# Kernel tuning notes

Hardware: AMD Instinct MI355X
Metric: run time of the kernel (lower is better)

Reference implementation:

```python
import jax, jax.numpy as jnp
import numpy as np


def _make_hadamard(n: int) -> np.ndarray:
    # Sylvester construction; H is symmetric so H == H.T
    H = np.array([[1.0]], dtype=np.float32)
    while H.shape[0] < n:
        H = np.block([[H, H], [H, -H]])
    return H


def setup_inputs() -> dict:
    key = jax.random.key(0)
    k1, k2, k3 = jax.random.split(key, 3)
    B, L, N = 64, 4096, 512  # N = num_features = num_features_pad (power of 2)
    x = jax.random.normal(k1, (B, L, N), dtype=jnp.float32)
    v = jax.random.uniform(k2, (N,), dtype=jnp.float32)  # torch.rand init
    T = jax.random.uniform(k3, (N,), dtype=jnp.float32)  # SoftThresholding threshold
    return {"x": x, "v": v, "T": T}


def reference(x, v, T):
    n = x.shape[-1]
    H = jnp.asarray(_make_hadamard(n))  # [n, n], symmetric
    scale = np.float32(1.0 / np.sqrt(n))
    # normalized Hadamard transform along last axis (dense-GEMM form, H.T == H)
    f1 = (x @ H) * scale
    # per-feature gate
    f2 = v * f1
    # soft-threshold: sign(x) * relu(|x| - T)
    f3 = jnp.sign(f2) * jax.nn.relu(jnp.abs(f2) - T)
    # inverse (same normalized) transform
    f4 = (f3 @ H) * scale
    # no padding (n is a power of 2), slice is identity; residual add
    return f4 + x
```

## Files before the change

### kernel.cpp

```cpp
#include <hip/hip_runtime.h>

#define NF 512
#define SCALE 0.044194173824159216f

#if defined(__has_builtin)
#  if __has_builtin(__builtin_amdgcn_permlane32_swap)
#    define HAVE_PL32 1
#  else
#    define HAVE_PL32 0
#  endif
#  if __has_builtin(__builtin_amdgcn_permlane16_swap)
#    define HAVE_PL16 1
#  else
#    define HAVE_PL16 0
#  endif
#else
#  define HAVE_PL32 0
#  define HAVE_PL16 0
#endif

typedef unsigned uint2v __attribute__((ext_vector_type(2)));
typedef float f32x4 __attribute__((ext_vector_type(4)));

template<int CTRL>
__device__ __forceinline__ float dppf(float x) {
    const int xi = __float_as_int(x);
    return __int_as_float(__builtin_amdgcn_update_dpp(xi, xi, CTRL, 0xF, 0xF, true));
}

template<int PAT>
__device__ __forceinline__ float swzf(float x) {
    return __int_as_float(__builtin_amdgcn_ds_swizzle(__float_as_int(x), PAT));
}

#if HAVE_PL16
__device__ __forceinline__ void bfly16(float& a, float& b) {
    uint2v t = __builtin_amdgcn_permlane16_swap(__float_as_uint(a), __float_as_uint(b), false, false);
    const float lo = __uint_as_float(t[0]);
    const float hi = __uint_as_float(t[1]);
    const float s = lo + hi;
    const float d = lo - hi;
    uint2v u = __builtin_amdgcn_permlane16_swap(__float_as_uint(s), __float_as_uint(d), false, false);
    a = __uint_as_float(u[0]);
    b = __uint_as_float(u[1]);
}
#endif

#if HAVE_PL32
__device__ __forceinline__ void bfly32(float& a, float& b) {
    uint2v t = __builtin_amdgcn_permlane32_swap(__float_as_uint(a), __float_as_uint(b), false, false);
    const float lo = __uint_as_float(t[0]);
    const float hi = __uint_as_float(t[1]);
    const float s = lo + hi;
    const float d = lo - hi;
    uint2v u = __builtin_amdgcn_permlane32_swap(__float_as_uint(s), __float_as_uint(d), false, false);
    a = __uint_as_float(u[0]);
    b = __uint_as_float(u[1]);
}
#endif

__device__ __forceinline__ void wht512(float r[8], const float sg1, const float sg2,
                                       const float sg4, const float sg8, const float sg16,
                                       const float sg32) {
    (void)sg16; (void)sg32;
#pragma unroll
    for (int s = 1; s < 8; s <<= 1) {
#pragma unroll
        for (int j = 0; j < 8; ++j) {
            if (!(j & s)) {
                const float u = r[j], w = r[j | s];
                r[j] = u + w;
                r[j | s] = u - w;
            }
        }
    }
#pragma unroll
    for (int j = 0; j < 8; ++j) { const float p = dppf<0xB1>(r[j]); r[j] = fmaf(sg1, r[j], p); }
#pragma unroll
    for (int j = 0; j < 8; ++j) { const float p = dppf<0x4E>(r[j]); r[j] = fmaf(sg2, r[j], p); }
#pragma unroll
    for (int j = 0; j < 8; ++j) { const float p = swzf<0x101F>(r[j]); r[j] = fmaf(sg4, r[j], p); }
#pragma unroll
    for (int j = 0; j < 8; ++j) { const float p = dppf<0x128>(r[j]); r[j] = fmaf(sg8, r[j], p); }
#if HAVE_PL16
#pragma unroll
    for (int j = 0; j < 8; j += 2) bfly16(r[j], r[j + 1]);
#else
#pragma unroll
    for (int j = 0; j < 8; ++j) { const float p = swzf<0x401F>(r[j]); r[j] = fmaf(sg16, r[j], p); }
#endif
#if HAVE_PL32
#pragma unroll
    for (int j = 0; j < 8; j += 2) bfly32(r[j], r[j + 1]);
#else
#pragma unroll
    for (int j = 0; j < 8; ++j) { const float p = __shfl_xor(r[j], 32, 64); r[j] = fmaf(sg32, r[j], p); }
#endif
}

__global__ __launch_bounds__(256, 4)
void wht512_soft_kernel(const float* __restrict__ x,
                        const float* __restrict__ gate,
                        const float* __restrict__ thr,
                        float* __restrict__ out,
                        const int nrows) {
    const int lane = threadIdx.x & 63;
    const int wave = blockIdx.x * (blockDim.x >> 6) + (threadIdx.x >> 6);
    const int nwaves = gridDim.x * (blockDim.x >> 6);

    const float sg1  = (lane & 1)  ? -1.0f : 1.0f;
    const float sg2  = (lane & 2)  ? -1.0f : 1.0f;
    const float sg4  = (lane & 4)  ? -1.0f : 1.0f;
    const float sg8  = (lane & 8)  ? -1.0f : 1.0f;
    const float sg16 = (lane & 16) ? -1.0f : 1.0f;
    const float sg32 = (lane & 32) ? -1.0f : 1.0f;

    float vg[8], tg[8];
    {
        const f32x4 a = ((const f32x4*)gate)[lane * 2];
        const f32x4 b = ((const f32x4*)gate)[lane * 2 + 1];
        vg[0] = a.x * SCALE; vg[1] = a.y * SCALE; vg[2] = a.z * SCALE; vg[3] = a.w * SCALE;
        vg[4] = b.x * SCALE; vg[5] = b.y * SCALE; vg[6] = b.z * SCALE; vg[7] = b.w * SCALE;
        const f32x4 c = ((const f32x4*)thr)[lane * 2];
        const f32x4 d = ((const f32x4*)thr)[lane * 2 + 1];
        tg[0] = c.x; tg[1] = c.y; tg[2] = c.z; tg[3] = c.w;
        tg[4] = d.x; tg[5] = d.y; tg[6] = d.z; tg[7] = d.w;
    }

    int row = wave;
    f32x4 ca, cb;
    if (row < nrows) {
        const f32x4* xr = (const f32x4*)(x + (size_t)row * NF);
        ca = __builtin_nontemporal_load(&xr[lane * 2]);
        cb = __builtin_nontemporal_load(&xr[lane * 2 + 1]);
    }

    for (; row < nrows; row += nwaves) {
        const int nrow = row + nwaves;
        f32x4 na = ca, nb = cb;
        if (nrow < nrows) {
            const f32x4* xn = (const f32x4*)(x + (size_t)nrow * NF);
            na = __builtin_nontemporal_load(&xn[lane * 2]);
            nb = __builtin_nontemporal_load(&xn[lane * 2 + 1]);
        }

        float r[8] = {ca.x, ca.y, ca.z, ca.w, cb.x, cb.y, cb.z, cb.w};

        wht512(r, sg1, sg2, sg4, sg8, sg16, sg32);

#pragma unroll
        for (int j = 0; j < 8; ++j) {
            const float f = r[j] * vg[j];
            const float mdiff = fabsf(f) - tg[j];
            r[j] = (mdiff > 0.0f) ? copysignf(mdiff, f) : 0.0f;
        }

        wht512(r, sg1, sg2, sg4, sg8, sg16, sg32);

        f32x4 oa, ob;
        oa.x = fmaf(r[0], SCALE, ca.x);
        oa.y = fmaf(r[1], SCALE, ca.y);
        oa.z = fmaf(r[2], SCALE, ca.z);
        oa.w = fmaf(r[3], SCALE, ca.w);
        ob.x = fmaf(r[4], SCALE, cb.x);
        ob.y = fmaf(r[5], SCALE, cb.y);
        ob.z = fmaf(r[6], SCALE, cb.z);
        ob.w = fmaf(r[7], SCALE, cb.w);
        f32x4* orow = (f32x4*)(out + (size_t)row * NF);
        __builtin_nontemporal_store(oa, &orow[lane * 2]);
        __builtin_nontemporal_store(ob, &orow[lane * 2 + 1]);

        ca = na;
        cb = nb;
    }
}

extern "C" void kernel_launch(void* const* d_in, const int* in_sizes, int n_in,
                              void* d_out, int out_size, void* d_ws, size_t ws_size,
                              hipStream_t stream) {
    const float* x = (const float*)d_in[0];
    const float* v = (const float*)d_in[1];
    const float* T = (const float*)d_in[2];
    float* out = (float*)d_out;

    const int nrows = in_sizes[0] / NF;

    dim3 block(256);
    dim3 grid(4096);
    hipLaunchKernelGGL(wht512_soft_kernel, grid, block, 0, stream, x, v, T, out, nrows);
}
```

Measured before the change: 235.1 us.

## Process two rows per wave with interleaved butterflies and plain loads/stores

Each wave now handles a pair of adjacent rows and interleaves their Hadamard butterfly and cross-lane stages. This raises instruction-level parallelism, hides DPP/permlane latency, and doubles the bytes in flight per wave. Nontemporal loads and stores are also replaced with ordinary ones. The cost is higher register pressure, and an odd final row would be dropped, though the row count here is even.

```diff
diff --git a/kernel.cpp b/kernel.cpp
--- a/kernel.cpp
+++ b/kernel.cpp
@@ -59,42 +59,74 @@
 }
 #endif
 
-__device__ __forceinline__ void wht512(float r[8], const float sg1, const float sg2,
-                                       const float sg4, const float sg8, const float sg16,
-                                       const float sg32) {
+__device__ __forceinline__ void wht512_pair(float a[8], float b[8],
+                                            const float sg1, const float sg2,
+                                            const float sg4, const float sg8,
+                                            const float sg16, const float sg32) {
     (void)sg16; (void)sg32;
 #pragma unroll
     for (int s = 1; s < 8; s <<= 1) {
 #pragma unroll
         for (int j = 0; j < 8; ++j) {
             if (!(j & s)) {
-                const float u = r[j], w = r[j | s];
-                r[j] = u + w;
-                r[j | s] = u - w;
+                const float ua = a[j], wa = a[j | s];
+                const float ub = b[j], wb = b[j | s];
+                a[j] = ua + wa; a[j | s] = ua - wa;
+                b[j] = ub + wb; b[j | s] = ub - wb;
             }
         }
     }
 #pragma unroll
-    for (int j = 0; j < 8; ++j) { const float p = dppf<0xB1>(r[j]); r[j] = fmaf(sg1, r[j], p); }
-#pragma unroll
-    for (int j = 0; j < 8; ++j) { const float p = dppf<0x4E>(r[j]); r[j] = fmaf(sg2, r[j], p); }
-#pragma unroll
-    for (int j = 0; j < 8; ++j) { const float p = swzf<0x101F>(r[j]); r[j] = fmaf(sg4, r[j], p); }
-#pragma unroll
-    for (int j = 0; j < 8; ++j) { const float p = dppf<0x128>(r[j]); r[j] = fmaf(sg8, r[j], p); }
+    for (int j = 0; j < 8; ++j) {
+        const float pa = dppf<0xB1>(a[j]);
+        const float pb = dppf<0xB1>(b[j]);
+        a[j] = fmaf(sg1, a[j], pa);
+        b[j] = fmaf(sg1, b[j], pb);
+    }
+#pragma unroll
+    for (int j = 0; j < 8; ++j) {
+        const float pa = dppf<0x4E>(a[j]);
+        const float pb = dppf<0x4E>(b[j]);
+        a[j] = fmaf(sg2, a[j], pa);
+        b[j] = fmaf(sg2, b[j], pb);
+    }
+#pragma unroll
+    for (int j = 0; j < 8; ++j) {
+        const float pa = swzf<0x101F>(a[j]);
+        const float pb = swzf<0x101F>(b[j]);
+        a[j] = fmaf(sg4, a[j], pa);
+        b[j] = fmaf(sg4, b[j], pb);
+    }
+#pragma unroll
+    for (int j = 0; j < 8; ++j) {
+        const float pa = dppf<0x128>(a[j]);
+        const float pb = dppf<0x128>(b[j]);
+        a[j] = fmaf(sg8, a[j], pa);
+        b[j] = fmaf(sg8, b[j], pb);
+    }
 #if HAVE_PL16
 #pragma unroll
-    for (int j = 0; j < 8; j += 2) bfly16(r[j], r[j + 1]);
+    for (int j = 0; j < 8; j += 2) { bfly16(a[j], a[j + 1]); bfly16(b[j], b[j + 1]); }
 #else
 #pragma unroll
-    for (int j = 0; j < 8; ++j) { const float p = swzf<0x401F>(r[j]); r[j] = fmaf(sg16, r[j], p); }
+    for (int j = 0; j < 8; ++j) {
+        const float pa = swzf<0x401F>(a[j]);
+        const float pb = swzf<0x401F>(b[j]);
+        a[j] = fmaf(sg16, a[j], pa);
+        b[j] = fmaf(sg16, b[j], pb);
+    }
 #endif
 #if HAVE_PL32
 #pragma unroll
-    for (int j = 0; j < 8; j += 2) bfly32(r[j], r[j + 1]);
+    for (int j = 0; j < 8; j += 2) { bfly32(a[j], a[j + 1]); bfly32(b[j], b[j + 1]); }
 #else
 #pragma unroll
-    for (int j = 0; j < 8; ++j) { const float p = __shfl_xor(r[j], 32, 64); r[j] = fmaf(sg32, r[j], p); }
+    for (int j = 0; j < 8; ++j) {
+        const float pa = __shfl_xor(a[j], 32, 64);
+        const float pb = __shfl_xor(b[j], 32, 64);
+        a[j] = fmaf(sg32, a[j], pa);
+        b[j] = fmaf(sg32, b[j], pb);
+    }
 #endif
 }
 
@@ -107,6 +139,7 @@
     const int lane = threadIdx.x & 63;
     const int wave = blockIdx.x * (blockDim.x >> 6) + (threadIdx.x >> 6);
     const int nwaves = gridDim.x * (blockDim.x >> 6);
+    const int npairs = nrows >> 1;
 
     const float sg1  = (lane & 1)  ? -1.0f : 1.0f;
     const float sg2  = (lane & 2)  ? -1.0f : 1.0f;
@@ -127,51 +160,61 @@
         tg[4] = d.x; tg[5] = d.y; tg[6] = d.z; tg[7] = d.w;
     }
 
-    int row = wave;
-    f32x4 ca, cb;
-    if (row < nrows) {
-        const f32x4* xr = (const f32x4*)(x + (size_t)row * NF);
-        ca = __builtin_nontemporal_load(&xr[lane * 2]);
-        cb = __builtin_nontemporal_load(&xr[lane * 2 + 1]);
-    }
-
-    for (; row < nrows; row += nwaves) {
-        const int nrow = row + nwaves;
-        f32x4 na = ca, nb = cb;
-        if (nrow < nrows) {
-            const f32x4* xn = (const f32x4*)(x + (size_t)nrow * NF);
-            na = __builtin_nontemporal_load(&xn[lane * 2]);
-            nb = __builtin_nontemporal_load(&xn[lane * 2 + 1]);
+    int pr = wave;
+    f32x4 c0a, c0b, c1a, c1b;
+    if (pr < npairs) {
+        const f32x4* x0 = (const f32x4*)(x + (size_t)(2 * pr) * NF);
+        c0a = x0[lane * 2];
+        c0b = x0[lane * 2 + 1];
+        c1a = x0[128 + lane * 2];
+        c1b = x0[128 + lane * 2 + 1];
+    }
+
+    for (; pr < npairs; pr += nwaves) {
+        const int npr = pr + nwaves;
+        f32x4 n0a = c0a, n0b = c0b, n1a = c1a, n1b = c1b;
+        if (npr < npairs) {
+            const f32x4* xn = (const f32x4*)(x + (size_t)(2 * npr) * NF);
+            n0a = xn[lane * 2];
+            n0b = xn[lane * 2 + 1];
+            n1a = xn[128 + lane * 2];
+            n1b = xn[128 + lane * 2 + 1];
         }
 
-        float r[8] = {ca.x, ca.y, ca.z, ca.w, cb.x, cb.y, cb.z, cb.w};
-
-        wht512(r, sg1, sg2, sg4, sg8, sg16, sg32);
+        float r0[8] = {c0a.x, c0a.y, c0a.z, c0a.w, c0b.x, c0b.y, c0b.z, c0b.w};
+        float r1[8] = {c1a.x, c1a.y, c1a.z, c1a.w, c1b.x, c1b.y, c1b.z, c1b.w};
+
+        wht512_pair(r0, r1, sg1, sg2, sg4, sg8, sg16, sg32);
 
 #pragma unroll
         for (int j = 0; j < 8; ++j) {
-            const float f = r[j] * vg[j];
-            const float mdiff = fabsf(f) - tg[j];
-            r[j] = (mdiff > 0.0f) ? copysignf(mdiff, f) : 0.0f;
+            const float f0 = r0[j] * vg[j];
+            const float f1 = r1[j] * vg[j];
+            const float m0 = fabsf(f0) - tg[j];
+            const float m1 = fabsf(f1) - tg[j];
+            r0[j] = (m0 > 0.0f) ? copysignf(m0, f0) : 0.0f;
+            r1[j] = (m1 > 0.0f) ? copysignf(m1, f1) : 0.0f;
         }
 
-        wht512(r, sg1, sg2, sg4, sg8, sg16, sg32);
-
-        f32x4 oa, ob;
-        oa.x = fmaf(r[0], SCALE, ca.x);
-        oa.y = fmaf(r[1], SCALE, ca.y);
-        oa.z = fmaf(r[2], SCALE, ca.z);
-        oa.w = fmaf(r[3], SCALE, ca.w);
-        ob.x = fmaf(r[4], SCALE, cb.x);
-        ob.y = fmaf(r[5], SCALE, cb.y);
-        ob.z = fmaf(r[6], SCALE, cb.z);
-        ob.w = fmaf(r[7], SCALE, cb.w);
-        f32x4* orow = (f32x4*)(out + (size_t)row * NF);
-        __builtin_nontemporal_store(oa, &orow[lane * 2]);
-        __builtin_nontemporal_store(ob, &orow[lane * 2 + 1]);
-
-        ca = na;
-        cb = nb;
+        wht512_pair(r0, r1, sg1, sg2, sg4, sg8, sg16, sg32);
+
+        f32x4 o0a, o0b, o1a, o1b;
+        o0a.x = fmaf(r0[0], SCALE, c0a.x); o0a.y = fmaf(r0[1], SCALE, c0a.y);
+        o0a.z = fmaf(r0[2], SCALE, c0a.z); o0a.w = fmaf(r0[3], SCALE, c0a.w);
+        o0b.x = fmaf(r0[4], SCALE, c0b.x); o0b.y = fmaf(r0[5], SCALE, c0b.y);
+        o0b.z = fmaf(r0[6], SCALE, c0b.z); o0b.w = fmaf(r0[7], SCALE, c0b.w);
+        o1a.x = fmaf(r1[0], SCALE, c1a.x); o1a.y = fmaf(r1[1], SCALE, c1a.y);
+        o1a.z = fmaf(r1[2], SCALE, c1a.z); o1a.w = fmaf(r1[3], SCALE, c1a.w);
+        o1b.x = fmaf(r1[4], SCALE, c1b.x); o1b.y = fmaf(r1[5], SCALE, c1b.y);
+        o1b.z = fmaf(r1[6], SCALE, c1b.z); o1b.w = fmaf(r1[7], SCALE, c1b.w);
+
+        f32x4* orow = (f32x4*)(out + (size_t)(2 * pr) * NF);
+        orow[lane * 2]           = o0a;
+        orow[lane * 2 + 1]       = o0b;
+        orow[128 + lane * 2]     = o1a;
+        orow[128 + lane * 2 + 1] = o1b;
+
+        c0a = n0a; c0b = n0b; c1a = n1a; c1b = n1b;
     }
 }
 
```

Result: faster. 205.1 us (-12.8%).
